# Kernel tuning notes

Measured on AMD Instinct MI355X. Metric: run time of the kernel, lower is better.

The kernel has to match this reference:

```python
import jax, jax.numpy as jnp
import numpy as np

U = 256
B = 128
D = 256  # input_size


def _outer(a, b):
    # a,b: [B,U] -> [B,U,U]
    return a[:, :, None] * b[:, None, :]


def _hadamard_sigma(s1, s2, m1, m2):
    # sigma1*sigma2 + diag(m1) s2 diag(m1) + diag(m2) s1 diag(m2)
    return s1 * s2 + _outer(m1, m1) * s2 + _outer(m2, m2) * s1


def _w_t_Sigma_w(W, S):
    # W: [U,U], S: [B,U,U] -> W^T S W
    return jnp.einsum('ji,bjk,kl->bil', W, S, W)


def _x_Sigma_w_x_T(x, W_Sigma):
    # sum(x*x) scalar per batch times W_Sigma
    return jnp.sum(x * x, axis=1)[:, None, None] * W_Sigma


def _tr_Sigma(S, W_Sigma):
    return jnp.trace(S, axis1=1, axis2=2)[:, None, None] * W_Sigma


def setup_inputs() -> dict:
    key = jax.random.key(0)
    ks = jax.random.split(key, 16)
    inp = {
        'inputs': jax.random.normal(ks[0], (B, D), jnp.float32),
        'prev_state': jax.random.normal(ks[1], (B, U), jnp.float32),
        'Sigma_state': jax.random.normal(ks[2], (B, U, U), jnp.float32) * 0.05,
        'U_z': jax.random.normal(ks[3], (D, U), jnp.float32) * 0.05,
        'uz_sigma': jax.random.uniform(ks[4], (U,), jnp.float32, -12.0, -2.2),
        'W_z': jax.random.normal(ks[5], (U, U), jnp.float32) * 0.05,
        'wz_sigma': jax.random.uniform(ks[6], (U,), jnp.float32, -12.0, -2.2),
        'U_r': jax.random.normal(ks[7], (D, U), jnp.float32) * 0.05,
        'ur_sigma': jax.random.uniform(ks[8], (U,), jnp.float32, -12.0, -2.2),
        'W_r': jax.random.normal(ks[9], (U, U), jnp.float32) * 0.05,
        'wr_sigma': jax.random.uniform(ks[10], (U,), jnp.float32, -12.0, -2.2),
        'U_h': jax.random.normal(ks[11], (D, U), jnp.float32) * 0.05,
        'uh_sigma': jax.random.uniform(ks[12], (U,), jnp.float32, -12.0, -2.2),
        'W_h': jax.random.normal(ks[13], (U, U), jnp.float32) * 0.05,
        'wh_sigma': jax.random.uniform(ks[14], (U,), jnp.float32, -12.0, -2.2),
    }
    return inp


def reference(inputs, prev_state, Sigma_state, U_z, uz_sigma, W_z, wz_sigma,
              U_r, ur_sigma, W_r, wr_sigma, U_h, uh_sigma, W_h, wh_sigma):
    # z gate
    mz = inputs @ U_z + prev_state @ W_z
    z = jax.nn.sigmoid(mz)
    Uz_S = jnp.diag(jax.nn.softplus(uz_sigma))
    Wz_S = jnp.diag(jax.nn.softplus(wz_sigma))
    Sigma_zz = (_w_t_Sigma_w(W_z, Sigma_state)
                + _x_Sigma_w_x_T(prev_state, Wz_S)
                + _tr_Sigma(Sigma_state, Wz_S)
                + _x_Sigma_w_x_T(inputs, Uz_S))
    gz = z * (1.0 - z)  # d sigmoid
    Sigma_z = Sigma_zz * _outer(gz, gz)

    # r gate
    mr = inputs @ U_r + prev_state @ W_r
    r = jax.nn.sigmoid(mr)
    Ur_S = jnp.diag(jax.nn.softplus(ur_sigma))
    Wr_S = jnp.diag(jax.nn.softplus(wr_sigma))
    Sigma_rr = (_w_t_Sigma_w(W_r, Sigma_state)
                + _x_Sigma_w_x_T(prev_state, Wr_S)
                + _tr_Sigma(Sigma_state, Wr_S)
                + _x_Sigma_w_x_T(inputs, Ur_S))
    gr = r * (1.0 - r)
    Sigma_r = Sigma_rr * _outer(gr, gr)

    # candidate h
    sr = prev_state * r
    mh = inputs @ U_h + sr @ W_h
    h = jnp.tanh(mh)
    Uh_S = jnp.diag(jax.nn.softplus(uh_sigma))
    Wh_S = jnp.diag(jax.nn.softplus(wh_sigma))
    sigma_g = _hadamard_sigma(Sigma_state, Sigma_r, prev_state, r)
    Sigma_hh = (_w_t_Sigma_w(W_h, sigma_g)
                + _x_Sigma_w_x_T(sr, Wh_S)
                + _tr_Sigma(sigma_g, Wh_S)
                + _x_Sigma_w_x_T(inputs, Uh_S))
    gh = 1.0 - h * h  # d tanh
    Sigma_h = Sigma_hh * _outer(gh, gh)

    # output mean and covariance
    mu_out = z * prev_state + (1.0 - z) * h
    sigma_a = _hadamard_sigma(Sigma_z, Sigma_state, z, prev_state)
    sigma_b = _hadamard_sigma(Sigma_z, Sigma_h, 1.0 - z, h)
    sigma_ab = Sigma_z * _outer(prev_state, h)
    sigma_abT = Sigma_z * _outer(h, prev_state)
    Sigma_out = sigma_a + sigma_b - sigma_ab - sigma_abT
    return mu_out, Sigma_out
```

## Files before the change

kernel.cpp:

```cpp
#include <hip/hip_runtime.h>
#include <math.h>


typedef __attribute__((ext_vector_type(8))) short sh8;
typedef __attribute__((ext_vector_type(4))) float f4;
typedef __attribute__((ext_vector_type(4))) unsigned short us4;

__device__ __forceinline__ unsigned short f2bf(float f) {
  unsigned int u = __float_as_uint(f);
  u = (u + 0x7fffu + ((u >> 16) & 1u)) >> 16;
  return (unsigned short)u;
}
__device__ __forceinline__ float bf2f(unsigned short u) {
  return __uint_as_float(((unsigned int)u) << 16);
}
__device__ __forceinline__ f4 mfma16(sh8 a, sh8 b, f4 c) {
  return __builtin_amdgcn_mfma_f32_16x16x32_bf16(a, b, c, 0, 0, 0);
}


__global__ __launch_bounds__(256) void prep_kernel(
    const float* __restrict__ xin, const float* __restrict__ prev,
    const float* __restrict__ S,
    const float* __restrict__ Uz, const float* __restrict__ Wz,
    const float* __restrict__ uzs, const float* __restrict__ wzs,
    const float* __restrict__ Ur, const float* __restrict__ Wr,
    const float* __restrict__ urs, const float* __restrict__ wrs,
    const float* __restrict__ Uh, const float* __restrict__ Wh,
    const float* __restrict__ uhs, const float* __restrict__ whs,
    unsigned short* __restrict__ Sfrag, unsigned short* __restrict__ packs,
    float* __restrict__ spzw, float* __restrict__ spzu,
    float* __restrict__ sprw, float* __restrict__ spru,
    float* __restrict__ sphw, float* __restrict__ sphu,
    float* __restrict__ sxA, float* __restrict__ spA, float* __restrict__ trSA,
    float* __restrict__ zv, float* __restrict__ rv,
    float* __restrict__ gzv, float* __restrict__ grv)
{
  const int blk = blockIdx.x, t = threadIdx.x;
  __shared__ float Srows[16][260];
  __shared__ float xs[256], ps[256];

  if (blk < 2048) {
    const int b = blk >> 4, R = blk & 15;
    const float* Sb = S + ((size_t)b << 16) + (size_t)(R * 16) * 256;
#pragma unroll
    for (int i = 0; i < 4; ++i) {
      int e = t + i * 256;
      int row = e >> 6, c4 = e & 63;
      f4 v = reinterpret_cast<const f4*>(Sb)[e];
      *reinterpret_cast<f4*>(&Srows[row][c4 * 4]) = v;
    }
    __syncthreads();
    unsigned short* outb = Sfrag + ((size_t)b << 16) + R * 512;
#pragma unroll
    for (int qi = 0; qi < 2; ++qi) {
      int q = t + qi * 256;
      int kt = q >> 6, lane = q & 63;
      int l15 = lane & 15, c0 = kt * 32 + (lane >> 4) * 8;
      union { unsigned short u[8]; uint4 v; } pk;
#pragma unroll
      for (int e = 0; e < 8; ++e) pk.u[e] = f2bf(Srows[l15][c0 + e]);
      *reinterpret_cast<uint4*>(outb + kt * 8192 + lane * 8) = pk.v;
    }
    return;
  }

  if (blk < 2096) {
    int gid = (blk - 2048) * 256 + t;
#pragma unroll
    for (int q2 = 0; q2 < 4; ++q2) {
      int cid = gid * 4 + q2;
      int p = cid >> 13, c = cid & 8191;
      const float* W = (p >> 1) == 0 ? Wz : ((p >> 1) == 1 ? Wr : Wh);
      int lane = c & 63, l15 = lane & 15, lhi = lane >> 4;
      int n, k8;
      if ((p & 1) == 0) {
        int nb = (c >> 11) & 3, kt = (c >> 8) & 7, ct = (c >> 6) & 3;
        n = nb * 64 + ct * 16 + l15; k8 = kt * 32 + lhi * 8;
      } else {
        int wv = (c >> 11) & 3, rt = (c >> 9) & 3, jt = (c >> 6) & 7;
        n = wv * 64 + rt * 16 + l15; k8 = jt * 32 + lhi * 8;
      }
      union { unsigned short u[8]; uint4 v; } pk;
#pragma unroll
      for (int e = 0; e < 8; ++e) pk.u[e] = f2bf(W[(k8 + e) * 256 + n]);
      *reinterpret_cast<uint4*>(packs + (size_t)p * 65536 + (size_t)c * 8) = pk.v;
    }
    return;
  }

  if (blk < 2224) {
    const int b = blk - 2096;
    __shared__ float red[12];
    float x = xin[b * 256 + t];
    float p = prev[b * 256 + t];
    float d = S[(size_t)b * 65536 + (size_t)t * 257];
    float a0 = x * x, a1 = p * p, a2 = d;
#pragma unroll
    for (int off = 32; off; off >>= 1) {
      a0 += __shfl_down(a0, off, 64);
      a1 += __shfl_down(a1, off, 64);
      a2 += __shfl_down(a2, off, 64);
    }
    if ((t & 63) == 0) {
      int w = t >> 6;
      red[w] = a0; red[4 + w] = a1; red[8 + w] = a2;
    }
    __syncthreads();
    if (t == 0) {
      sxA[b] = red[0] + red[1] + red[2] + red[3];
      spA[b] = red[4] + red[5] + red[6] + red[7];
      trSA[b] = red[8] + red[9] + red[10] + red[11];
    }
    return;
  }

  if (blk == 2224) {
    spzw[t] = log1pf(expf(wzs[t])); spzu[t] = log1pf(expf(uzs[t]));
    sprw[t] = log1pf(expf(wrs[t])); spru[t] = log1pf(expf(urs[t]));
    sphw[t] = log1pf(expf(whs[t])); sphu[t] = log1pf(expf(uhs[t]));
    return;
  }

  const int q = blk - 2225, g = q >> 7, b = q & 127;
  xs[t] = xin[b * 256 + t];
  ps[t] = prev[b * 256 + t];
  __syncthreads();
  const float* U = g ? Ur : Uz;
  const float* W = g ? Wr : Wz;
  float a0 = 0.f, a1 = 0.f, a2 = 0.f, a3 = 0.f;
  for (int k = 0; k < 256; k += 4) {
    a0 = fmaf(xs[k],     U[(k)     * 256 + t], a0);
    a1 = fmaf(xs[k + 1], U[(k + 1) * 256 + t], a1);
    a2 = fmaf(xs[k + 2], U[(k + 2) * 256 + t], a2);
    a3 = fmaf(xs[k + 3], U[(k + 3) * 256 + t], a3);
  }
  for (int k = 0; k < 256; k += 4) {
    a0 = fmaf(ps[k],     W[(k)     * 256 + t], a0);
    a1 = fmaf(ps[k + 1], W[(k + 1) * 256 + t], a1);
    a2 = fmaf(ps[k + 2], W[(k + 2) * 256 + t], a2);
    a3 = fmaf(ps[k + 3], W[(k + 3) * 256 + t], a3);
  }
  const float m = (a0 + a1) + (a2 + a3);
  const float zz = 1.f / (1.f + expf(-m));
  const int idx = b * 256 + t;
  if (g == 0) { zv[idx] = zz; gzv[idx] = zz * (1.f - zz); }
  else        { rv[idx] = zz; grv[idx] = zz * (1.f - zz); }
}

__global__ __launch_bounds__(256) void fuse_kernel(
    const float* __restrict__ xin, const float* __restrict__ prev,
    const float* __restrict__ S,
    const float* __restrict__ Uh, const float* __restrict__ Wh,
    const float* __restrict__ zv, const float* __restrict__ rv,
    const float* __restrict__ gzv, const float* __restrict__ grv,
    const unsigned short* __restrict__ packs,
    const unsigned short* __restrict__ Sfrag,
    const float* __restrict__ spzw, const float* __restrict__ spzu,
    const float* __restrict__ sprw, const float* __restrict__ spru,
    const float* __restrict__ sxA, const float* __restrict__ spA,
    const float* __restrict__ trSA,
    unsigned short* __restrict__ Szbf, unsigned short* __restrict__ sgf,
    float* __restrict__ trsgP,
    float* __restrict__ ghv, float* __restrict__ pmhv,
    float* __restrict__ muOut, float* __restrict__ ssrA)
{
  __shared__ unsigned short Tt[64][264];
  __shared__ float ev0[256], evd[256], ev2[256], ev3[256];

  const int blk = blockIdx.x, tid = threadIdx.x;
  const f4 z4 = {0.f, 0.f, 0.f, 0.f};

  if (blk < 128) {
    float* xs  = (float*)&Tt[0][0];
    float* ps  = xs + 256;
    float* srs = ps + 256;
    float* red = srs + 256;
    const int b = blk, t = tid;
    xs[t] = xin[b * 256 + t];
    float pv = prev[b * 256 + t];
    ps[t] = pv;
    srs[t] = pv * rv[b * 256 + t];
    __syncthreads();
    float a0 = 0.f, a1 = 0.f, a2 = 0.f, a3 = 0.f;
    for (int k = 0; k < 256; k += 4) {
      a0 = fmaf(xs[k],     Uh[(k)     * 256 + t], a0);
      a1 = fmaf(xs[k + 1], Uh[(k + 1) * 256 + t], a1);
      a2 = fmaf(xs[k + 2], Uh[(k + 2) * 256 + t], a2);
      a3 = fmaf(xs[k + 3], Uh[(k + 3) * 256 + t], a3);
    }
    for (int k = 0; k < 256; k += 4) {
      a0 = fmaf(srs[k],     Wh[(k)     * 256 + t], a0);
      a1 = fmaf(srs[k + 1], Wh[(k + 1) * 256 + t], a1);
      a2 = fmaf(srs[k + 2], Wh[(k + 2) * 256 + t], a2);
      a3 = fmaf(srs[k + 3], Wh[(k + 3) * 256 + t], a3);
    }
    const float m = (a0 + a1) + (a2 + a3);
    const float h = tanhf(m);
    const int idx = b * 256 + t;
    const float z = zv[idx];
    ghv[idx]  = 1.f - h * h;
    pmhv[idx] = pv - h;
    muOut[idx] = z * pv + (1.f - z) * h;
    float s = srs[t] * srs[t];
#pragma unroll
    for (int off = 32; off; off >>= 1) s += __shfl_down(s, off, 64);
    __syncthreads();
    if ((t & 63) == 0) red[t >> 6] = s;
    __syncthreads();
    if (t == 0) ssrA[b] = red[0] + red[1] + red[2] + red[3];
    return;
  }

  const int q = blk - 128;
  const int c = q & 7, role = (q >> 3) & 7, chunk = q >> 6;
  const int b = chunk * 8 + c;
  const int isR = role >> 2, nb = role & 3, col0 = nb * 64;
  const int wave = tid >> 6, lane = tid & 63, lhi = lane >> 4, l15 = lane & 15;
  const size_t bb = (size_t)b << 16;
  const unsigned short* p1 = packs + (size_t)(isR ? 2 : 0) * 65536;
  const unsigned short* p2 = packs + (size_t)(isR ? 3 : 1) * 65536;

  {
    const int u = tid;
    const float sd = spA[b] + trSA[b], sx = sxA[b];
    if (isR) {
      ev0[u] = grv[b * 256 + u];
      evd[u] = sd * sprw[u] + sx * spru[u];
      ev2[u] = prev[b * 256 + u];
      ev3[u] = rv[b * 256 + u];
    } else {
      ev0[u] = gzv[b * 256 + u];
      evd[u] = sd * spzw[u] + sx * spzu[u];
    }
  }

  f4 acc[4][4];
#pragma unroll
  for (int i = 0; i < 4; ++i)
#pragma unroll
    for (int j = 0; j < 4; ++j) acc[i][j] = z4;

  const unsigned short* Af = Sfrag + bb;
#pragma unroll
  for (int kt = 0; kt < 8; ++kt) {
    sh8 af[4], bfr[4];
#pragma unroll
    for (int rt = 0; rt < 4; ++rt)
      af[rt] = *reinterpret_cast<const sh8*>(
          Af + kt * 8192 + (wave * 4 + rt) * 512 + lane * 8);
#pragma unroll
    for (int ct = 0; ct < 4; ++ct)
      bfr[ct] = *reinterpret_cast<const sh8*>(
          p1 + ((size_t)(((nb * 8 + kt) * 4 + ct) * 64 + lane) << 3));
#pragma unroll
    for (int rt = 0; rt < 4; ++rt)
#pragma unroll
      for (int ct = 0; ct < 4; ++ct)
        acc[rt][ct] = mfma16(af[rt], bfr[ct], acc[rt][ct]);
  }

#pragma unroll
  for (int rt = 0; rt < 4; ++rt) {
    const int row0 = wave * 64 + rt * 16 + lhi * 4;
#pragma unroll
    for (int ct = 0; ct < 4; ++ct) {
      const int cc = ct * 16 + l15;
      us4 p4;
      p4[0] = f2bf(acc[rt][ct][0]); p4[1] = f2bf(acc[rt][ct][1]);
      p4[2] = f2bf(acc[rt][ct][2]); p4[3] = f2bf(acc[rt][ct][3]);
      *reinterpret_cast<us4*>(&Tt[cc][row0]) = p4;
    }
  }
  __syncthreads();

#pragma unroll
  for (int i = 0; i < 4; ++i)
#pragma unroll
    for (int j = 0; j < 4; ++j) acc[i][j] = z4;

#pragma unroll
  for (int jt = 0; jt < 8; ++jt) {
    const int j8 = jt * 32 + lhi * 8;
    sh8 af[4], bfr[4];
#pragma unroll
    for (int rt = 0; rt < 4; ++rt)
      af[rt] = *reinterpret_cast<const sh8*>(
          p2 + ((size_t)(((wave * 4 + rt) * 8 + jt) * 64 + lane) << 3));
#pragma unroll
    for (int ct = 0; ct < 4; ++ct)
      bfr[ct] = *reinterpret_cast<const sh8*>(&Tt[ct * 16 + l15][j8]);
#pragma unroll
    for (int rt = 0; rt < 4; ++rt)
#pragma unroll
      for (int ct = 0; ct < 4; ++ct)
        acc[rt][ct] = mfma16(af[rt], bfr[ct], acc[rt][ct]);
  }

  float trloc = 0.f;
#pragma unroll
  for (int rt = 0; rt < 4; ++rt) {
    const int i0 = wave * 64 + rt * 16 + lhi * 4;
#pragma unroll
    for (int ct = 0; ct < 4; ++ct) {
      const int j = col0 + ct * 16 + l15;
#pragma unroll
      for (int rr = 0; rr < 4; ++rr) {
        const int i = i0 + rr;
        const size_t idx = bb + ((size_t)i << 8) + j;
        float Y = acc[rt][ct][rr] + ((i == j) ? evd[i] : 0.f);
        if (!isR) {
          Szbf[idx] = f2bf(Y * ev0[i] * ev0[j]);
        } else {
          float Sr = Y * ev0[i] * ev0[j];
          float Sv = S[idx];
          float sgv = Sr * (Sv + ev2[i] * ev2[j]) + ev3[i] * ev3[j] * Sv;
          size_t fo = bb + (size_t)((j >> 5) * 8192) + (size_t)((i >> 4) * 512)
                    + (size_t)((((j >> 3) & 3) * 16 + (i & 15)) * 8) + (j & 7);
          sgf[fo] = f2bf(sgv);
          if (i == j) trloc += sgv;
        }
      }
    }
  }

  if (isR) {
    if (wave == nb) {
#pragma unroll
      for (int off = 32; off; off >>= 1) trloc += __shfl_down(trloc, off, 64);
      if (lane == 0) trsgP[b * 4 + nb] = trloc;
    }
  }
}

__global__ __launch_bounds__(256) void gateh_kernel(
    const float* __restrict__ S,
    const unsigned short* __restrict__ sgf,
    const unsigned short* __restrict__ packs,
    const unsigned short* __restrict__ Szb,
    const float* __restrict__ ghv, const float* __restrict__ zv,
    const float* __restrict__ pmhv,
    const float* __restrict__ sphw, const float* __restrict__ sphu,
    const float* __restrict__ sxA, const float* __restrict__ ssrA,
    const float* __restrict__ trsgIn,
    float* __restrict__ fOut)
{
  __shared__ unsigned short Tt[64][264];
  __shared__ float ev0[256], evd[256], ev2[256], ev3[256];

  const int blk = blockIdx.x, tid = threadIdx.x;
  const int wave = tid >> 6, lane = tid & 63, lhi = lane >> 4, l15 = lane & 15;
  const int c = blk & 7, nb = (blk >> 3) & 3, chunk = blk >> 5;
  const int b = chunk * 8 + c, col0 = nb * 64;
  const size_t bb = (size_t)b << 16;
  const f4 z4 = {0.f, 0.f, 0.f, 0.f};
  const unsigned short* p1 = packs + (size_t)4 * 65536;
  const unsigned short* p2 = packs + (size_t)5 * 65536;

  {
    const int u = tid;
    float trsg = trsgIn[b * 4] + trsgIn[b * 4 + 1]
               + trsgIn[b * 4 + 2] + trsgIn[b * 4 + 3];
    ev0[u] = ghv[b * 256 + u];
    evd[u] = (ssrA[b] + trsg) * sphw[u] + sxA[b] * sphu[u];
    ev2[u] = zv[b * 256 + u];
    ev3[u] = pmhv[b * 256 + u];
  }

  f4 acc[4][4];
#pragma unroll
  for (int i = 0; i < 4; ++i)
#pragma unroll
    for (int j = 0; j < 4; ++j) acc[i][j] = z4;

  const unsigned short* Af = sgf + bb;
#pragma unroll
  for (int kt = 0; kt < 8; ++kt) {
    sh8 af[4], bfr[4];
#pragma unroll
    for (int rt = 0; rt < 4; ++rt)
      af[rt] = *reinterpret_cast<const sh8*>(
          Af + kt * 8192 + (wave * 4 + rt) * 512 + lane * 8);
#pragma unroll
    for (int ct = 0; ct < 4; ++ct)
      bfr[ct] = *reinterpret_cast<const sh8*>(
          p1 + ((size_t)(((nb * 8 + kt) * 4 + ct) * 64 + lane) << 3));
#pragma unroll
    for (int rt = 0; rt < 4; ++rt)
#pragma unroll
      for (int ct = 0; ct < 4; ++ct)
        acc[rt][ct] = mfma16(af[rt], bfr[ct], acc[rt][ct]);
  }

#pragma unroll
  for (int rt = 0; rt < 4; ++rt) {
    const int row0 = wave * 64 + rt * 16 + lhi * 4;
#pragma unroll
    for (int ct = 0; ct < 4; ++ct) {
      const int cc = ct * 16 + l15;
      us4 p4;
      p4[0] = f2bf(acc[rt][ct][0]); p4[1] = f2bf(acc[rt][ct][1]);
      p4[2] = f2bf(acc[rt][ct][2]); p4[3] = f2bf(acc[rt][ct][3]);
      *reinterpret_cast<us4*>(&Tt[cc][row0]) = p4;
    }
  }
  __syncthreads();

#pragma unroll
  for (int i = 0; i < 4; ++i)
#pragma unroll
    for (int j = 0; j < 4; ++j) acc[i][j] = z4;

#pragma unroll
  for (int jt = 0; jt < 8; ++jt) {
    const int j8 = jt * 32 + lhi * 8;
    sh8 af[4], bfr[4];
#pragma unroll
    for (int rt = 0; rt < 4; ++rt)
      af[rt] = *reinterpret_cast<const sh8*>(
          p2 + ((size_t)(((wave * 4 + rt) * 8 + jt) * 64 + lane) << 3));
#pragma unroll
    for (int ct = 0; ct < 4; ++ct)
      bfr[ct] = *reinterpret_cast<const sh8*>(&Tt[ct * 16 + l15][j8]);
#pragma unroll
    for (int rt = 0; rt < 4; ++rt)
#pragma unroll
      for (int ct = 0; ct < 4; ++ct)
        acc[rt][ct] = mfma16(af[rt], bfr[ct], acc[rt][ct]);
  }

#pragma unroll
  for (int rt = 0; rt < 4; ++rt) {
    const int i0 = wave * 64 + rt * 16 + lhi * 4;
#pragma unroll
    for (int ct = 0; ct < 4; ++ct) {
      const int j = col0 + ct * 16 + l15;
#pragma unroll
      for (int rr = 0; rr < 4; ++rr) {
        const int i = i0 + rr;
        const size_t idx = bb + ((size_t)i << 8) + j;
        float Sh = (acc[rt][ct][rr] + ((i == j) ? evd[i] : 0.f)) * ev0[i] * ev0[j];
        float Sv = S[idx];
        float Szv = bf2f(Szb[idx]);
        fOut[idx] = Szv * (Sv + Sh + ev3[i] * ev3[j])
                  + Sv * ev2[i] * ev2[j]
                  + Sh * (1.f - ev2[i]) * (1.f - ev2[j]);
      }
    }
  }
}

extern "C" void kernel_launch(void* const* d_in, const int* in_sizes, int n_in,
                              void* d_out, int out_size, void* d_ws, size_t ws_size,
                              hipStream_t stream)
{
  const float* xin  = (const float*)d_in[0];
  const float* prev = (const float*)d_in[1];
  const float* S    = (const float*)d_in[2];
  const float* Uz = (const float*)d_in[3];  const float* uzs = (const float*)d_in[4];
  const float* Wz = (const float*)d_in[5];  const float* wzs = (const float*)d_in[6];
  const float* Ur = (const float*)d_in[7];  const float* urs = (const float*)d_in[8];
  const float* Wr = (const float*)d_in[9];  const float* wrs = (const float*)d_in[10];
  const float* Uh = (const float*)d_in[11]; const float* uhs = (const float*)d_in[12];
  const float* Wh = (const float*)d_in[13]; const float* whs = (const float*)d_in[14];

  float* muOut  = (float*)d_out;
  float* SigOut = muOut + 128 * 256;

  char* p = (char*)d_ws;
  auto take = [&](size_t bytes) { void* q = (void*)p; p += bytes; return q; };
  unsigned short* Sfrag = (unsigned short*)take(16777216);
  unsigned short* sgf   = (unsigned short*)take(16777216);
  unsigned short* Szbf  = (unsigned short*)take(16777216);
  unsigned short* packs = (unsigned short*)take(786432);
  float* zv   = (float*)take(131072);
  float* rv   = (float*)take(131072);
  float* gzv  = (float*)take(131072);
  float* grv  = (float*)take(131072);
  float* ghv  = (float*)take(131072);
  float* pmhv = (float*)take(131072);
  float* spzw = (float*)take(1024);
  float* spzu = (float*)take(1024);
  float* sprw = (float*)take(1024);
  float* spru = (float*)take(1024);
  float* sphw = (float*)take(1024);
  float* sphu = (float*)take(1024);
  float* sxA  = (float*)take(512);
  float* spA  = (float*)take(512);
  float* trSA = (float*)take(512);
  float* ssrA = (float*)take(512);
  float* trsgP = (float*)take(2048);
  (void)in_sizes; (void)n_in; (void)out_size; (void)ws_size;

  prep_kernel<<<2481, 256, 0, stream>>>(
      xin, prev, S, Uz, Wz, uzs, wzs, Ur, Wr, urs, wrs, Uh, Wh, uhs, whs,
      Sfrag, packs, spzw, spzu, sprw, spru, sphw, sphu,
      sxA, spA, trSA, zv, rv, gzv, grv);

  fuse_kernel<<<1152, 256, 0, stream>>>(
      xin, prev, S, Uh, Wh, zv, rv, gzv, grv, packs, Sfrag,
      spzw, spzu, sprw, spru, sxA, spA, trSA,
      Szbf, sgf, trsgP, ghv, pmhv, muOut, ssrA);

  gateh_kernel<<<512, 256, 0, stream>>>(
      S, sgf, packs, Szbf, ghv, zv, pmhv, sphw, sphu,
      sxA, ssrA, trsgP, SigOut);
}
```

Before: 109.1 us.

## Merge z and r gate covariance blocks to share Sigma fragment loads

Each workgroup in the fused covariance kernel now computes both the z-gate and r-gate W^T S W tiles for one batch and column block, instead of separate blocks per gate. The Sigma_state A-fragments are loaded once and feed two accumulator sets, which halves the number of reads of that input, and the grid shrinks from 1152 to 640 blocks. In exchange each block doubles its accumulator registers and LDS use, which can lower occupancy. The launch bound now requests 2 blocks per CU.

```diff
diff --git a/kernel.cpp b/kernel.cpp
--- a/kernel.cpp
+++ b/kernel.cpp
@@ -148,7 +148,7 @@
   else        { rv[idx] = zz; grv[idx] = zz * (1.f - zz); }
 }
 
-__global__ __launch_bounds__(256) void fuse_kernel(
+__global__ __launch_bounds__(256, 2) void fuse_kernel(
     const float* __restrict__ xin, const float* __restrict__ prev,
     const float* __restrict__ S,
     const float* __restrict__ Uh, const float* __restrict__ Wh,
@@ -165,14 +165,16 @@
     float* __restrict__ ghv, float* __restrict__ pmhv,
     float* __restrict__ muOut, float* __restrict__ ssrA)
 {
-  __shared__ unsigned short Tt[64][264];
-  __shared__ float ev0[256], evd[256], ev2[256], ev3[256];
+  __shared__ unsigned short Ttz[64][264];
+  __shared__ unsigned short Ttr[64][264];
+  __shared__ float ev0z[256], evdz[256], ev0r[256], evdr[256];
+  __shared__ float ev2[256], ev3[256];
 
   const int blk = blockIdx.x, tid = threadIdx.x;
   const f4 z4 = {0.f, 0.f, 0.f, 0.f};
 
   if (blk < 128) {
-    float* xs  = (float*)&Tt[0][0];
+    float* xs  = (float*)&Ttz[0][0];
     float* ps  = xs + 256;
     float* srs = ps + 256;
     float* red = srs + 256;
@@ -213,51 +215,54 @@
   }
 
   const int q = blk - 128;
-  const int c = q & 7, role = (q >> 3) & 7, chunk = q >> 6;
+  const int c = q & 7, nb = (q >> 3) & 3, chunk = q >> 5;
   const int b = chunk * 8 + c;
-  const int isR = role >> 2, nb = role & 3, col0 = nb * 64;
+  const int col0 = nb * 64;
   const int wave = tid >> 6, lane = tid & 63, lhi = lane >> 4, l15 = lane & 15;
   const size_t bb = (size_t)b << 16;
-  const unsigned short* p1 = packs + (size_t)(isR ? 2 : 0) * 65536;
-  const unsigned short* p2 = packs + (size_t)(isR ? 3 : 1) * 65536;
+  const unsigned short* p1z = packs;
+  const unsigned short* p2z = packs + (size_t)1 * 65536;
+  const unsigned short* p1r = packs + (size_t)2 * 65536;
+  const unsigned short* p2r = packs + (size_t)3 * 65536;
 
   {
     const int u = tid;
     const float sd = spA[b] + trSA[b], sx = sxA[b];
-    if (isR) {
-      ev0[u] = grv[b * 256 + u];
-      evd[u] = sd * sprw[u] + sx * spru[u];
-      ev2[u] = prev[b * 256 + u];
-      ev3[u] = rv[b * 256 + u];
-    } else {
-      ev0[u] = gzv[b * 256 + u];
-      evd[u] = sd * spzw[u] + sx * spzu[u];
-    }
-  }
-
-  f4 acc[4][4];
+    ev0z[u] = gzv[b * 256 + u];
+    evdz[u] = sd * spzw[u] + sx * spzu[u];
+    ev0r[u] = grv[b * 256 + u];
+    evdr[u] = sd * sprw[u] + sx * spru[u];
+    ev2[u]  = prev[b * 256 + u];
+    ev3[u]  = rv[b * 256 + u];
+  }
+
+  f4 az[4][4], ar[4][4];
 #pragma unroll
   for (int i = 0; i < 4; ++i)
 #pragma unroll
-    for (int j = 0; j < 4; ++j) acc[i][j] = z4;
+    for (int j = 0; j < 4; ++j) { az[i][j] = z4; ar[i][j] = z4; }
 
   const unsigned short* Af = Sfrag + bb;
 #pragma unroll
   for (int kt = 0; kt < 8; ++kt) {
-    sh8 af[4], bfr[4];
+    sh8 af[4], bz[4], br[4];
 #pragma unroll
     for (int rt = 0; rt < 4; ++rt)
       af[rt] = *reinterpret_cast<const sh8*>(
           Af + kt * 8192 + (wave * 4 + rt) * 512 + lane * 8);
 #pragma unroll
-    for (int ct = 0; ct < 4; ++ct)
-      bfr[ct] = *reinterpret_cast<const sh8*>(
-          p1 + ((size_t)(((nb * 8 + kt) * 4 + ct) * 64 + lane) << 3));
-#pragma unroll
-    for (int rt = 0; rt < 4; ++rt)
-#pragma unroll
-      for (int ct = 0; ct < 4; ++ct)
-        acc[rt][ct] = mfma16(af[rt], bfr[ct], acc[rt][ct]);
+    for (int ct = 0; ct < 4; ++ct) {
+      const size_t po = (size_t)(((nb * 8 + kt) * 4 + ct) * 64 + lane) << 3;
+      bz[ct] = *reinterpret_cast<const sh8*>(p1z + po);
+      br[ct] = *reinterpret_cast<const sh8*>(p1r + po);
+    }
+#pragma unroll
+    for (int rt = 0; rt < 4; ++rt)
+#pragma unroll
+      for (int ct = 0; ct < 4; ++ct) {
+        az[rt][ct] = mfma16(af[rt], bz[ct], az[rt][ct]);
+        ar[rt][ct] = mfma16(af[rt], br[ct], ar[rt][ct]);
+      }
   }
 
 #pragma unroll
@@ -266,10 +271,13 @@
 #pragma unroll
     for (int ct = 0; ct < 4; ++ct) {
       const int cc = ct * 16 + l15;
-      us4 p4;
-      p4[0] = f2bf(acc[rt][ct][0]); p4[1] = f2bf(acc[rt][ct][1]);
-      p4[2] = f2bf(acc[rt][ct][2]); p4[3] = f2bf(acc[rt][ct][3]);
-      *reinterpret_cast<us4*>(&Tt[cc][row0]) = p4;
+      us4 pz, pr;
+      pz[0] = f2bf(az[rt][ct][0]); pz[1] = f2bf(az[rt][ct][1]);
+      pz[2] = f2bf(az[rt][ct][2]); pz[3] = f2bf(az[rt][ct][3]);
+      pr[0] = f2bf(ar[rt][ct][0]); pr[1] = f2bf(ar[rt][ct][1]);
+      pr[2] = f2bf(ar[rt][ct][2]); pr[3] = f2bf(ar[rt][ct][3]);
+      *reinterpret_cast<us4*>(&Ttz[cc][row0]) = pz;
+      *reinterpret_cast<us4*>(&Ttr[cc][row0]) = pr;
     }
   }
   __syncthreads();
@@ -277,24 +285,30 @@
 #pragma unroll
   for (int i = 0; i < 4; ++i)
 #pragma unroll
-    for (int j = 0; j < 4; ++j) acc[i][j] = z4;
+    for (int j = 0; j < 4; ++j) { az[i][j] = z4; ar[i][j] = z4; }
 
 #pragma unroll
   for (int jt = 0; jt < 8; ++jt) {
     const int j8 = jt * 32 + lhi * 8;
-    sh8 af[4], bfr[4];
-#pragma unroll
-    for (int rt = 0; rt < 4; ++rt)
-      af[rt] = *reinterpret_cast<const sh8*>(
-          p2 + ((size_t)(((wave * 4 + rt) * 8 + jt) * 64 + lane) << 3));
-#pragma unroll
-    for (int ct = 0; ct < 4; ++ct)
-      bfr[ct] = *reinterpret_cast<const sh8*>(&Tt[ct * 16 + l15][j8]);
-#pragma unroll
-    for (int rt = 0; rt < 4; ++rt)
-#pragma unroll
-      for (int ct = 0; ct < 4; ++ct)
-        acc[rt][ct] = mfma16(af[rt], bfr[ct], acc[rt][ct]);
+    sh8 a2z[4], a2r[4], bz[4], br[4];
+#pragma unroll
+    for (int rt = 0; rt < 4; ++rt) {
+      const size_t po = (size_t)(((wave * 4 + rt) * 8 + jt) * 64 + lane) << 3;
+      a2z[rt] = *reinterpret_cast<const sh8*>(p2z + po);
+      a2r[rt] = *reinterpret_cast<const sh8*>(p2r + po);
+    }
+#pragma unroll
+    for (int ct = 0; ct < 4; ++ct) {
+      bz[ct] = *reinterpret_cast<const sh8*>(&Ttz[ct * 16 + l15][j8]);
+      br[ct] = *reinterpret_cast<const sh8*>(&Ttr[ct * 16 + l15][j8]);
+    }
+#pragma unroll
+    for (int rt = 0; rt < 4; ++rt)
+#pragma unroll
+      for (int ct = 0; ct < 4; ++ct) {
+        az[rt][ct] = mfma16(a2z[rt], bz[ct], az[rt][ct]);
+        ar[rt][ct] = mfma16(a2r[rt], br[ct], ar[rt][ct]);
+      }
   }
 
   float trloc = 0.f;
@@ -308,28 +322,24 @@
       for (int rr = 0; rr < 4; ++rr) {
         const int i = i0 + rr;
         const size_t idx = bb + ((size_t)i << 8) + j;
-        float Y = acc[rt][ct][rr] + ((i == j) ? evd[i] : 0.f);
-        if (!isR) {
-          Szbf[idx] = f2bf(Y * ev0[i] * ev0[j]);
-        } else {
-          float Sr = Y * ev0[i] * ev0[j];
-          float Sv = S[idx];
-          float sgv = Sr * (Sv + ev2[i] * ev2[j]) + ev3[i] * ev3[j] * Sv;
-          size_t fo = bb + (size_t)((j >> 5) * 8192) + (size_t)((i >> 4) * 512)
-                    + (size_t)((((j >> 3) & 3) * 16 + (i & 15)) * 8) + (j & 7);
-          sgf[fo] = f2bf(sgv);
-          if (i == j) trloc += sgv;
-        }
+        float Yz = az[rt][ct][rr] + ((i == j) ? evdz[i] : 0.f);
+        Szbf[idx] = f2bf(Yz * ev0z[i] * ev0z[j]);
+        float Yr = ar[rt][ct][rr] + ((i == j) ? evdr[i] : 0.f);
+        float Sr = Yr * ev0r[i] * ev0r[j];
+        float Sv = S[idx];
+        float sgv = Sr * (Sv + ev2[i] * ev2[j]) + ev3[i] * ev3[j] * Sv;
+        size_t fo = bb + (size_t)((j >> 5) * 8192) + (size_t)((i >> 4) * 512)
+                  + (size_t)((((j >> 3) & 3) * 16 + (i & 15)) * 8) + (j & 7);
+        sgf[fo] = f2bf(sgv);
+        if (i == j) trloc += sgv;
       }
     }
   }
 
-  if (isR) {
-    if (wave == nb) {
-#pragma unroll
-      for (int off = 32; off; off >>= 1) trloc += __shfl_down(trloc, off, 64);
-      if (lane == 0) trsgP[b * 4 + nb] = trloc;
-    }
+  if (wave == nb) {
+#pragma unroll
+    for (int off = 32; off; off >>= 1) trloc += __shfl_down(trloc, off, 64);
+    if (lane == 0) trsgP[b * 4 + nb] = trloc;
   }
 }
 
@@ -497,7 +507,7 @@
       Sfrag, packs, spzw, spzu, sprw, spru, sphw, sphu,
       sxA, spA, trSA, zv, rv, gzv, grv);
 
-  fuse_kernel<<<1152, 256, 0, stream>>>(
+  fuse_kernel<<<640, 256, 0, stream>>>(
       xin, prev, S, Uh, Wh, zv, rv, gzv, grv, packs, Sfrag,
       spzw, spzu, sprw, spru, sxA, spA, trSA,
       Szbf, sgf, trsgP, ghv, pmhv, muOut, ssrA);
```

Result: faster. 90.69 us (-16.9%).
